# Kernel optimization log

Hardware: AMD Instinct MI355X
Metric: run time of the kernel (lower is better)

Reference implementation:

```python
import jax, jax.numpy as jnp
import numpy as np

B, N, D, H = 8, 1024, 512, 8
DK = D // H  # key_dim == val_dim == 64
LN_EPS = 1e-5


def setup_inputs() -> dict:
    key = jax.random.key(0)
    ks = jax.random.split(key, 16)
    stdv = 1.0 / np.sqrt(D)
    u = lambda k, shape, s: jax.random.uniform(k, shape, jnp.float32, -s, s)
    inp = {
        'q': jax.random.normal(ks[0], (B, N, D), jnp.float32),
        'mask': jax.random.uniform(ks[1], (B, N, N)) < 0.1,  # True = masked out
        # eps1 is torch.zeros in the source (never re-initialized); use small
        'eps1': jax.random.normal(ks[2], (D, D), jnp.float32) * 0.03,
        # 3 MLP layers, stacked on leading axis. Linear: y = x @ W.T + b
        'U_w': u(ks[3], (3, D, D), stdv), 'U_b': u(ks[4], (3, D), stdv),
        'V_w': u(ks[5], (3, D, D), stdv), 'V_b': u(ks[6], (3, D), stdv),
        'ln_g': jnp.ones((3, D), jnp.float32), 'ln_b': jnp.zeros((3, D), jnp.float32),
        'W_query': u(ks[7], (H, D, DK), 1.0 / np.sqrt(DK)),
        'W_key':   u(ks[8], (H, D, DK), 1.0 / np.sqrt(DK)),
        'W_val':   u(ks[9], (H, D, DK), 1.0 / np.sqrt(DK)),
        'W_out':   u(ks[10], (H, DK, D), stdv),
    }
    return inp


def _layer_norm(x, g, b):
    mu = jnp.mean(x, axis=-1, keepdims=True)
    var = jnp.mean(jnp.square(x - mu), axis=-1, keepdims=True)
    return (x - mu) * jax.lax.rsqrt(var + LN_EPS) * g + b


def _mlp_layer(x, Uw, Ub, Vw, Vb, g, b):
    # U1 -> (identity maxpool k=1) -> V1 -> LayerNorm -> ReLU -> residual
    y = x @ Uw.T + Ub
    y = y @ Vw.T + Vb
    y = _layer_norm(y, g, b)
    return x + jax.nn.relu(y)


def reference(q, mask, eps1, U_w, U_b, V_w, V_b, ln_g, ln_b,
              W_query, W_key, W_val, W_out):
    nf = 1.0 / np.sqrt(DK)  # norm_factor; applied to BOTH Q and K as in source
    h = q
    for l in range(3):
        h = _mlp_layer(h @ eps1, U_w[l], U_b[l], V_w[l], V_b[l], ln_g[l], ln_b[l])
    # per-head projections: (H,B,N,DK)
    Q = jnp.einsum('bqd,hdk->hbqk', q, W_query) * nf
    K = jnp.einsum('bgd,hdk->hbgk', h, W_key) * nf
    V = jnp.einsum('bgd,hdk->hbgk', h, W_val)
    scores = jnp.einsum('hbqk,hbgk->hbqg', Q, K)  # (H,B,N,N)
    scores = jnp.where(mask[None], -1e10, scores)
    attn = jax.nn.softmax(scores, axis=-1)
    heads = jnp.einsum('hbqg,hbgv->hbqv', attn, V)
    out = jnp.einsum('hbqv,hvd->bqd', heads, W_out)  # (B,N,D)
    return out
```

## Files before the change

kernel.cpp:

```cpp
#include <hip/hip_runtime.h>

typedef __attribute__((ext_vector_type(8))) short bhalf8;
typedef __attribute__((ext_vector_type(4))) float f32x4;

__device__ __forceinline__ ushort f2bf(float f) {
  unsigned u = __builtin_bit_cast(unsigned, f);
  unsigned r = u + 0x7fffu + ((u >> 16) & 1u);
  return (ushort)(r >> 16);
}

__device__ __forceinline__ void gld16(const ushort* g, ushort* l) {
  __builtin_amdgcn_global_load_lds((const __attribute__((address_space(1))) void*)g,
                                   (__attribute__((address_space(3))) void*)l, 16, 0, 0);
}

__global__ __launch_bounds__(256) void prep_kernel(
    const float* __restrict__ q, const int* __restrict__ mask,
    const float* __restrict__ eps1, const float* __restrict__ U_w,
    const float* __restrict__ V_w, const float* __restrict__ Wq,
    const float* __restrict__ Wk, const float* __restrict__ Wv,
    const float* __restrict__ Wo, const float* __restrict__ U_b,
    const float* __restrict__ V_b,
    ushort* __restrict__ qb, unsigned long long* __restrict__ mbits,
    ushort* __restrict__ uwb, ushort* __restrict__ vwb,
    ushort* __restrict__ e1b, ushort* __restrict__ e1t,
    ushort* __restrict__ wqkv, ushort* __restrict__ wot,
    float* __restrict__ cvec) {
  int i = blockIdx.x * 256 + threadIdx.x;
  if (i < 4194304) {
    qb[i] = f2bf(q[i]);
  } else if (i < 12582912) {
    int j = i - 4194304;
    unsigned long long bb = __ballot(mask[j] != 0);
    if ((threadIdx.x & 63) == 0) {
      int b = j >> 20, qq = (j >> 10) & 1023, g = j & 1023;
      mbits[((size_t)b * 16 + (g >> 6)) * 1024 + qq] = bb;
    }
  } else if (i < 13369344) {
    int j = i - 12582912;
    uwb[j] = f2bf(U_w[j]);
  } else if (i < 14155776) {
    int j = i - 13369344;
    vwb[j] = f2bf(V_w[j]);
  } else if (i < 14417920) {
    int j = i - 14155776;
    e1b[j] = f2bf(eps1[j]);
  } else if (i < 14680064) {
    int j = i - 14417920; int n = j >> 9, k = j & 511;
    e1t[j] = f2bf(eps1[k * 512 + n]);
  } else if (i < 15466496) {
    int j = i - 14680064; int n = j >> 9, d = j & 511;
    const float* W = (n < 512) ? Wq : (n < 1024 ? Wk : Wv);
    float sc = (n < 512) ? 0.02255252509f : 1.0f;
    int nl = n & 511;
    wqkv[j] = f2bf(W[((nl >> 6) * 512 + d) * 64 + (nl & 63)] * sc);
  } else if (i < 15728640) {
    int j = i - 15466496; int d = j >> 9, hv = j & 511;
    wot[j] = f2bf(Wo[hv * 512 + d]);
  } else {
    int j = i - 15728640;
    int idx = j >> 6, ln = j & 63;
    int l = idx >> 9;
    const float* vr = V_w + (size_t)idx * 512 + ln * 8;
    const float* ur = U_b + l * 512 + ln * 8;
    float s = 0;
#pragma unroll
    for (int t = 0; t < 8; t++) s += vr[t] * ur[t];
#pragma unroll
    for (int off = 1; off < 64; off <<= 1) s += __shfl_xor(s, off, 64);
    if (ln == 0) cvec[idx] = s + V_b[idx];
  }
}

__global__ __launch_bounds__(256) void mrepack_kernel(
    const unsigned long long* __restrict__ mbits,
    unsigned long long* __restrict__ mT) {
  int id = blockIdx.x * 4 + (threadIdx.x >> 6);
  int lane = threadIdx.x & 63;
  int b = id >> 8, gw = (id >> 4) & 15, qw = id & 15;
  unsigned long long row = mbits[((size_t)b * 16 + gw) * 1024 + qw * 64 + lane];
  unsigned long long keep = 0;
  for (int j = 0; j < 64; j++) {
    unsigned long long bal = __ballot((row >> j) & 1ull);
    if (lane == j) keep = bal;
  }
  mT[((size_t)b * 1024 + gw * 64 + lane) * 16 + qw] = keep;
}

template <int BN>
__global__ __launch_bounds__(256) void gemm_nt(
    const ushort* __restrict__ A0, const ushort* __restrict__ A1,
    const ushort* __restrict__ Bt0, const ushort* __restrict__ Bt1,
    int bsplit, int mstride, int M, int K,
    ushort* __restrict__ O0, const float* __restrict__ b0,
    ushort* __restrict__ O1, const float* __restrict__ b1,
    ushort* __restrict__ O2, const float* __restrict__ b2,
    float* __restrict__ F0, float* __restrict__ F1, int vtreg) {
  __shared__ ushort As[128 * 32];
  __shared__ ushort Bs[BN * 32];
  int tid = threadIdx.x;
  int wave = tid >> 6, lane = tid & 63;
  int quad = lane >> 4, col = lane & 15;
  int m0 = blockIdx.x * 128, n0 = blockIdx.y * BN;
  const ushort* A = (A1 && n0 >= 512) ? A1 : A0;
  const ushort* Bp = ((n0 < bsplit) ? Bt0 + (size_t)n0 * K
                                    : Bt1 + (size_t)(n0 - bsplit) * K) +
                     (size_t)(m0 >> 9) * mstride;
  constexpr int NI = BN / 32;
  int wm = (BN == 128) ? (wave >> 1) * 64 : (wave & 1) * 64;
  int wn = (BN == 128) ? (wave & 1) * 64 : (wave >> 1) * 32;
  f32x4 acc[4][NI] = {};
  int srow = wave * 16 + (lane >> 2);
  int skc = (lane & 3) * 8;
  const ushort* gA0 = A + (size_t)(m0 + srow) * K + skc;
  const ushort* gA1 = gA0 + (size_t)64 * K;
  const ushort* gB0 = Bp + (size_t)srow * K + skc;
  const ushort* gB1 = gB0 + (size_t)64 * K;
  ushort* lA0 = &As[wave * 16 * 32];
  ushort* lA1 = &As[(64 + wave * 16) * 32];
  ushort* lB0 = &Bs[wave * 16 * 32];
  ushort* lB1 = (BN == 128) ? &Bs[(64 + wave * 16) * 32] : nullptr;

  gld16(gA0, lA0);
  gld16(gA1, lA1);
  gld16(gB0, lB0);
  if (BN == 128) gld16(gB1, lB1);

  for (int k0 = 0; k0 < K; k0 += 32) {
    __syncthreads();
    bhalf8 af[4], bg[NI];
#pragma unroll
    for (int i = 0; i < 4; i++)
      af[i] = *(bhalf8*)&As[(wm + i * 16 + col) * 32 + quad * 8];
#pragma unroll
    for (int i = 0; i < NI; i++)
      bg[i] = *(bhalf8*)&Bs[(wn + i * 16 + col) * 32 + quad * 8];
    __syncthreads();
    if (k0 + 32 < K) {
      gld16(gA0 + k0 + 32, lA0);
      gld16(gA1 + k0 + 32, lA1);
      gld16(gB0 + k0 + 32, lB0);
      if (BN == 128) gld16(gB1 + k0 + 32, lB1);
    }
#pragma unroll
    for (int mi = 0; mi < 4; mi++)
#pragma unroll
      for (int ni = 0; ni < NI; ni++)
        acc[mi][ni] = __builtin_amdgcn_mfma_f32_16x16x32_bf16(af[mi], bg[ni], acc[mi][ni], 0, 0, 0);
  }

  int reg = n0 >> 9;
  ushort* Oreg = (reg == 0) ? O0 : (reg == 1 ? O1 : O2);
  const float* breg = (reg == 0) ? b0 : (reg == 1 ? b1 : b2);
  float* Freg = (reg == 0) ? F0 : (reg == 1 ? F1 : nullptr);
  bool vt = (reg == vtreg);
#pragma unroll
  for (int mi = 0; mi < 4; mi++)
#pragma unroll
    for (int ni = 0; ni < NI; ni++) {
      int cn = n0 + wn + ni * 16 + col;
      int cnl = cn & 511;
      int cmb = m0 + wm + mi * 16 + quad * 4;
      float bv = breg ? breg[cnl] : 0.f;
      if (vt) {
        ushort4 pk;
        pk.x = f2bf(acc[mi][ni][0] + bv);
        pk.y = f2bf(acc[mi][ni][1] + bv);
        pk.z = f2bf(acc[mi][ni][2] + bv);
        pk.w = f2bf(acc[mi][ni][3] + bv);
        *(ushort4*)&O2[((size_t)((cmb >> 10) * 512 + cnl)) * 1024 + (cmb & 1023)] = pk;
      } else if (Freg) {
#pragma unroll
        for (int r = 0; r < 4; r++)
          Freg[(size_t)(cmb + r) * 512 + cnl] = acc[mi][ni][r] + bv;
      } else {
#pragma unroll
        for (int r = 0; r < 4; r++)
          Oreg[(size_t)(cmb + r) * 512 + cnl] = f2bf(acc[mi][ni][r] + bv);
      }
    }
}

__global__ __launch_bounds__(256) void ln_kernel(
    const float* __restrict__ z, const ushort* __restrict__ tb,
    const float* __restrict__ lgam, const float* __restrict__ lbet,
    ushort* __restrict__ hb) {
  int row = blockIdx.x * 4 + (threadIdx.x >> 6);
  int lane = threadIdx.x & 63;
  int cbase = lane * 8;
  const float* zr = z + (size_t)row * 512 + cbase;
  float x[8];
  *(float4*)&x[0] = *(const float4*)zr;
  *(float4*)&x[4] = *(const float4*)(zr + 4);
  float sum = 0;
#pragma unroll
  for (int i = 0; i < 8; i++) sum += x[i];
#pragma unroll
  for (int off = 1; off < 64; off <<= 1) sum += __shfl_xor(sum, off, 64);
  float mu = sum * (1.f / 512.f);
  float vs = 0;
#pragma unroll
  for (int i = 0; i < 8; i++) { float d = x[i] - mu; vs += d * d; }
#pragma unroll
  for (int off = 1; off < 64; off <<= 1) vs += __shfl_xor(vs, off, 64);
  float rstd = rsqrtf(vs * (1.f / 512.f) + 1e-5f);
  uint4 tr = *(const uint4*)&tb[(size_t)row * 512 + cbase];
  float tv[8];
  {
    const unsigned* u = (const unsigned*)&tr;
#pragma unroll
    for (int w = 0; w < 4; w++) {
      tv[2 * w] = __builtin_bit_cast(float, u[w] << 16);
      tv[2 * w + 1] = __builtin_bit_cast(float, u[w] & 0xFFFF0000u);
    }
  }
  ushort outv[8];
#pragma unroll
  for (int i = 0; i < 8; i++) {
    float val = (x[i] - mu) * rstd * lgam[cbase + i] + lbet[cbase + i];
    outv[i] = f2bf(tv[i] + fmaxf(val, 0.f));
  }
  *(uint4*)&hb[(size_t)row * 512 + cbase] = *(uint4*)outv;
}

__global__ __launch_bounds__(256, 2) void attn_kernel(
    const ushort* __restrict__ Qp, const ushort* __restrict__ Kp,
    const ushort* __restrict__ VtG, const unsigned long long* __restrict__ mT,
    ushort* __restrict__ Op) {
  int bh = blockIdx.x, qt = blockIdx.y;
  int b = bh >> 3, h = bh & 7;
  __shared__ __align__(16) char pool[21504];
  int tid = threadIdx.x, wave = tid >> 6, lane = tid & 63;
  int quad = lane >> 4, col = lane & 15;
  int q0 = qt * 64;
  ushort* Ps = (ushort*)pool + wave * 2560;

  bhalf8 aq[4][2];
  {
    const ushort* qbase = &Qp[(size_t)(b * 1024 + q0 + col) * 512 + h * 64 + quad * 8];
#pragma unroll
    for (int qs = 0; qs < 4; qs++) {
      aq[qs][0] = *(const bhalf8*)(qbase + (size_t)(qs * 16) * 512);
      aq[qs][1] = *(const bhalf8*)(qbase + (size_t)(qs * 16) * 512 + 32);
    }
  }
  bhalf8 ones;
  {
    short v = (col == 0) ? (short)0x3F80 : (short)0;
#pragma unroll
    for (int j = 0; j < 8; j++) ones[j] = v;
  }
  f32x4 o[4][5] = {};
  const ushort* kbase = &Kp[(size_t)(b * 1024 + col) * 512 + h * 64 + quad * 8];
  const ushort* vbase = &VtG[(size_t)(bh * 64 + col) * 1024];
  int gsel = (quad >> 1) * 64 + (quad & 1) * 8;

  for (int g0 = 0; g0 < 1024; g0 += 128) {
    int gA = g0 + wave * 16;
    bhalf8 bk[2][2];
    bk[0][0] = *(const bhalf8*)(kbase + (size_t)gA * 512);
    bk[0][1] = *(const bhalf8*)(kbase + (size_t)gA * 512 + 32);
    bk[1][0] = *(const bhalf8*)(kbase + (size_t)(gA + 64) * 512);
    bk[1][1] = *(const bhalf8*)(kbase + (size_t)(gA + 64) * 512 + 32);
    bhalf8 bv[4];
#pragma unroll
    for (int vs = 0; vs < 4; vs++)
      bv[vs] = *(const bhalf8*)(vbase + (size_t)(vs * 16) * 1024 + g0 + wave * 16 + gsel);
    unsigned long long inv0 = ~(mT[(size_t)(b * 1024 + gA + col) * 16 + qt] >> (quad * 4));
    unsigned long long inv1 = ~(mT[(size_t)(b * 1024 + gA + 64 + col) * 16 + qt] >> (quad * 4));
    unsigned i0lo = (unsigned)inv0, i0hi = (unsigned)(inv0 >> 32);
    unsigned i1lo = (unsigned)inv1, i1hi = (unsigned)(inv1 >> 32);
#pragma unroll
    for (int qs = 0; qs < 4; qs++) {
      f32x4 s0 = {}, s1 = {};
      s0 = __builtin_amdgcn_mfma_f32_16x16x32_bf16(aq[qs][0], bk[0][0], s0, 0, 0, 0);
      s0 = __builtin_amdgcn_mfma_f32_16x16x32_bf16(aq[qs][1], bk[0][1], s0, 0, 0, 0);
      s1 = __builtin_amdgcn_mfma_f32_16x16x32_bf16(aq[qs][0], bk[1][0], s1, 0, 0, 0);
      s1 = __builtin_amdgcn_mfma_f32_16x16x32_bf16(aq[qs][1], bk[1][1], s1, 0, 0, 0);
      unsigned w0 = (qs < 2) ? i0lo : i0hi;
      unsigned w1 = (qs < 2) ? i1lo : i1hi;
#pragma unroll
      for (int r = 0; r < 4; r++) {
        int pos = (qs & 1) * 16 + r;
        unsigned k0 = (unsigned)((int)(w0 << (31 - pos)) >> 31);
        unsigned k1 = (unsigned)((int)(w1 << (31 - pos)) >> 31);
        unsigned p0 = __builtin_bit_cast(unsigned, __builtin_amdgcn_exp2f(s0[r])) & k0;
        unsigned p1 = __builtin_bit_cast(unsigned, __builtin_amdgcn_exp2f(s1[r])) & k1;
        Ps[(qs * 16 + quad * 4 + r) * 40 + col] = (ushort)((p0 + 0x8000u) >> 16);
        Ps[(qs * 16 + quad * 4 + r) * 40 + 16 + col] = (ushort)((p1 + 0x8000u) >> 16);
      }
    }
#pragma unroll
    for (int qs = 0; qs < 4; qs++) {
      bhalf8 ap = *(const bhalf8*)&Ps[(qs * 16 + col) * 40 + quad * 8];
#pragma unroll
      for (int vs = 0; vs < 4; vs++)
        o[qs][vs] = __builtin_amdgcn_mfma_f32_16x16x32_bf16(ap, bv[vs], o[qs][vs], 0, 0, 0);
      o[qs][4] = __builtin_amdgcn_mfma_f32_16x16x32_bf16(ap, ones, o[qs][4], 0, 0, 0);
    }
  }
  float* R = (float*)pool;
  for (int src = 1; src < 4; src++) {
    __syncthreads();
    if (wave == src) {
      float* dst = R + lane * 84;
#pragma unroll
      for (int qs = 0; qs < 4; qs++)
#pragma unroll
        for (int vs = 0; vs < 5; vs++)
          *(f32x4*)(dst + (qs * 5 + vs) * 4) = o[qs][vs];
    }
    __syncthreads();
    if (wave == 0) {
      const float* sp = R + lane * 84;
#pragma unroll
      for (int qs = 0; qs < 4; qs++)
#pragma unroll
        for (int vs = 0; vs < 5; vs++)
          o[qs][vs] += *(const f32x4*)(sp + (qs * 5 + vs) * 4);
    }
  }
  if (wave == 0) {
#pragma unroll
    for (int qs = 0; qs < 4; qs++) {
      float rl[4];
#pragma unroll
      for (int r = 0; r < 4; r++) {
        float lv = __shfl(o[qs][4][r], lane & 48, 64);
        rl[r] = __builtin_amdgcn_rcpf(lv);
      }
#pragma unroll
      for (int vs = 0; vs < 4; vs++)
#pragma unroll
        for (int r = 0; r < 4; r++) {
          int qrow = q0 + qs * 16 + quad * 4 + r;
          Op[(size_t)(b * 1024 + qrow) * 512 + h * 64 + vs * 16 + col] =
              f2bf(o[qs][vs][r] * rl[r]);
        }
    }
  }
}

extern "C" void kernel_launch(void* const* d_in, const int* in_sizes, int n_in,
                              void* d_out, int out_size, void* d_ws, size_t ws_size,
                              hipStream_t stream) {
  const float* q    = (const float*)d_in[0];
  const int*   mask = (const int*)d_in[1];
  const float* eps1 = (const float*)d_in[2];
  const float* U_w  = (const float*)d_in[3];
  const float* U_b  = (const float*)d_in[4];
  const float* V_w  = (const float*)d_in[5];
  const float* V_b  = (const float*)d_in[6];
  const float* ln_g = (const float*)d_in[7];
  const float* ln_b = (const float*)d_in[8];
  const float* Wq   = (const float*)d_in[9];
  const float* Wk   = (const float*)d_in[10];
  const float* Wv   = (const float*)d_in[11];
  const float* Wo   = (const float*)d_in[12];
  float* out = (float*)d_out;

  char* ws = (char*)d_ws;
  auto carve = [&](size_t bytes) { char* p = ws; ws += bytes; return p; };
  ushort* qb   = (ushort*)carve(8388608);
  ushort* uwb  = (ushort*)carve(1572864);
  ushort* vwb  = (ushort*)carve(1572864);
  ushort* e1b  = (ushort*)carve(524288);
  ushort* e1t  = (ushort*)carve(524288);
  ushort* wqkv = (ushort*)carve(1572864);
  ushort* wot  = (ushort*)carve(524288);
  ushort* A1b  = (ushort*)carve(1572864);
  ushort* Gtb  = (ushort*)carve(1572864);
  float*  cvec = (float*)carve(6144);
  unsigned long long* mbits = (unsigned long long*)carve(1048576);
  unsigned long long* mT    = (unsigned long long*)carve(2097152);
  ushort* tb   = (ushort*)carve(8388608);
  float*  zf   = (float*)carve(16777216);
  ushort* hb   = (ushort*)carve(8388608);
  ushort* Qb   = (ushort*)carve(8388608);
  ushort* Kb   = (ushort*)carve(8388608);
  ushort* VtG  = (ushort*)carve(8388608);
  ushort* Ob   = (ushort*)carve(8388608);
  const int BIG = 1 << 30;

  prep_kernel<<<61824, 256, 0, stream>>>(q, mask, eps1, U_w, V_w, Wq, Wk, Wv, Wo,
                                         U_b, V_b, qb, mbits, uwb, vwb, e1b, e1t,
                                         wqkv, wot, cvec);
  mrepack_kernel<<<512, 256, 0, stream>>>(mbits, mT);
  gemm_nt<128><<<dim3(4, 12), 256, 0, stream>>>(
      e1b, nullptr, uwb, nullptr, BIG, 0, 512, 512,
      A1b, nullptr, A1b + 262144, nullptr, A1b + 524288, nullptr,
      nullptr, nullptr, -1);
  gemm_nt<64><<<dim3(12, 8), 256, 0, stream>>>(
      vwb, nullptr, A1b, nullptr, BIG, 262144, 1536, 512,
      Gtb, nullptr, nullptr, nullptr, nullptr, nullptr,
      nullptr, nullptr, -1);
  const ushort* hsrc = qb;
  for (int l = 0; l < 3; l++) {
    gemm_nt<128><<<dim3(64, 8), 256, 0, stream>>>(
        hsrc, nullptr, e1t, Gtb + l * 262144, 512, 0, 8192, 512,
        tb, nullptr, nullptr, cvec + l * 512, nullptr, nullptr,
        nullptr, zf, -1);
    ln_kernel<<<2048, 256, 0, stream>>>(zf, tb, ln_g + l * 512, ln_b + l * 512, hb);
    hsrc = hb;
  }
  gemm_nt<128><<<dim3(64, 12), 256, 0, stream>>>(
      qb, hb, wqkv, nullptr, BIG, 0, 8192, 512,
      Qb, nullptr, Kb, nullptr, VtG, nullptr, nullptr, nullptr, 2);
  attn_kernel<<<dim3(64, 16), 256, 0, stream>>>(Qb, Kb, VtG, mT, Ob);
  gemm_nt<64><<<dim3(64, 8), 256, 0, stream>>>(
      Ob, nullptr, wot, nullptr, BIG, 0, 8192, 512,
      nullptr, nullptr, nullptr, nullptr, nullptr, nullptr, out, nullptr, -1);
}
```

Before: 318.5 us.

## Tile K/V/mask layouts for attention and widen GEMM k-step to 64

The GEMM epilogue now writes K and V directly into per-(batch,head) 16-row tiled layouts, so the attention kernel's fragment loads become contiguous per wave instead of strided across 512-wide rows. The mask repack stores pre-inverted bits in a q-tile-major layout to shrink and linearize the mask reads. The GEMM main loop moves to a 64-wide k-step with double the LDS tile, halving the barrier and issue count per K. Scattered epilogue stores for K and the larger LDS footprint are the trade-offs.

Result: no change. 321.4 us (+0.9%).

```diff
diff --git a/kernel.cpp b/kernel.cpp
--- a/kernel.cpp
+++ b/kernel.cpp
@@ -74,7 +74,7 @@
 
 __global__ __launch_bounds__(256) void mrepack_kernel(
     const unsigned long long* __restrict__ mbits,
-    unsigned long long* __restrict__ mT) {
+    unsigned long long* __restrict__ mT2) {
   int id = blockIdx.x * 4 + (threadIdx.x >> 6);
   int lane = threadIdx.x & 63;
   int b = id >> 8, gw = (id >> 4) & 15, qw = id & 15;
@@ -84,7 +84,7 @@
     unsigned long long bal = __ballot((row >> j) & 1ull);
     if (lane == j) keep = bal;
   }
-  mT[((size_t)b * 1024 + gw * 64 + lane) * 16 + qw] = keep;
+  mT2[((size_t)b * 16 + qw) * 1024 + gw * 64 + lane] = ~keep;
 }
 
 template <int BN>
@@ -95,9 +95,10 @@
     ushort* __restrict__ O0, const float* __restrict__ b0,
     ushort* __restrict__ O1, const float* __restrict__ b1,
     ushort* __restrict__ O2, const float* __restrict__ b2,
-    float* __restrict__ F0, float* __restrict__ F1, int vtreg) {
-  __shared__ ushort As[128 * 32];
-  __shared__ ushort Bs[BN * 32];
+    float* __restrict__ F0, float* __restrict__ F1,
+    int ktreg, int vtreg) {
+  __shared__ ushort As[128 * 64];
+  __shared__ ushort Bs[BN * 64];
   int tid = threadIdx.x;
   int wave = tid >> 6, lane = tid & 63;
   int quad = lane >> 4, col = lane & 15;
@@ -110,50 +111,72 @@
   int wm = (BN == 128) ? (wave >> 1) * 64 : (wave & 1) * 64;
   int wn = (BN == 128) ? (wave & 1) * 64 : (wave >> 1) * 32;
   f32x4 acc[4][NI] = {};
-  int srow = wave * 16 + (lane >> 2);
-  int skc = (lane & 3) * 8;
-  const ushort* gA0 = A + (size_t)(m0 + srow) * K + skc;
-  const ushort* gA1 = gA0 + (size_t)64 * K;
-  const ushort* gB0 = Bp + (size_t)srow * K + skc;
-  const ushort* gB1 = gB0 + (size_t)64 * K;
-  ushort* lA0 = &As[wave * 16 * 32];
-  ushort* lA1 = &As[(64 + wave * 16) * 32];
-  ushort* lB0 = &Bs[wave * 16 * 32];
-  ushort* lB1 = (BN == 128) ? &Bs[(64 + wave * 16) * 32] : nullptr;
-
-  gld16(gA0, lA0);
-  gld16(gA1, lA1);
-  gld16(gB0, lB0);
-  if (BN == 128) gld16(gB1, lB1);
-
-  for (int k0 = 0; k0 < K; k0 += 32) {
+  int srow = wave * 16 + (lane >> 3);
+  int skc = (lane & 7) * 8;
+  const ushort* gA = A + (size_t)(m0 + srow) * K + skc;
+  const ushort* gB = Bp + (size_t)srow * K + skc;
+  ushort* lA = &As[(wave * 16) * 64];
+  ushort* lB = &Bs[(wave * 16) * 64];
+  const size_t rK8 = (size_t)8 * K, rK64 = (size_t)64 * K;
+
+  gld16(gA, lA);
+  gld16(gA + rK8, lA + 8 * 64);
+  gld16(gA + rK64, lA + 64 * 64);
+  gld16(gA + rK64 + rK8, lA + 72 * 64);
+  gld16(gB, lB);
+  gld16(gB + rK8, lB + 8 * 64);
+  if (BN == 128) {
+    gld16(gB + rK64, lB + 64 * 64);
+    gld16(gB + rK64 + rK8, lB + 72 * 64);
+  }
+
+  for (int k0 = 0; k0 < K; k0 += 64) {
     __syncthreads();
     bhalf8 af[4], bg[NI];
 #pragma unroll
     for (int i = 0; i < 4; i++)
-      af[i] = *(bhalf8*)&As[(wm + i * 16 + col) * 32 + quad * 8];
+      af[i] = *(bhalf8*)&As[(wm + i * 16 + col) * 64 + quad * 8];
 #pragma unroll
     for (int i = 0; i < NI; i++)
-      bg[i] = *(bhalf8*)&Bs[(wn + i * 16 + col) * 32 + quad * 8];
-    __syncthreads();
-    if (k0 + 32 < K) {
-      gld16(gA0 + k0 + 32, lA0);
-      gld16(gA1 + k0 + 32, lA1);
-      gld16(gB0 + k0 + 32, lB0);
-      if (BN == 128) gld16(gB1 + k0 + 32, lB1);
-    }
+      bg[i] = *(bhalf8*)&Bs[(wn + i * 16 + col) * 64 + quad * 8];
 #pragma unroll
     for (int mi = 0; mi < 4; mi++)
 #pragma unroll
       for (int ni = 0; ni < NI; ni++)
         acc[mi][ni] = __builtin_amdgcn_mfma_f32_16x16x32_bf16(af[mi], bg[ni], acc[mi][ni], 0, 0, 0);
+    bhalf8 af2[4], bg2[NI];
+#pragma unroll
+    for (int i = 0; i < 4; i++)
+      af2[i] = *(bhalf8*)&As[(wm + i * 16 + col) * 64 + 32 + quad * 8];
+#pragma unroll
+    for (int i = 0; i < NI; i++)
+      bg2[i] = *(bhalf8*)&Bs[(wn + i * 16 + col) * 64 + 32 + quad * 8];
+    __syncthreads();
+    if (k0 + 64 < K) {
+      const ushort* a = gA + k0 + 64;
+      const ushort* b = gB + k0 + 64;
+      gld16(a, lA);
+      gld16(a + rK8, lA + 8 * 64);
+      gld16(a + rK64, lA + 64 * 64);
+      gld16(a + rK64 + rK8, lA + 72 * 64);
+      gld16(b, lB);
+      gld16(b + rK8, lB + 8 * 64);
+      if (BN == 128) {
+        gld16(b + rK64, lB + 64 * 64);
+        gld16(b + rK64 + rK8, lB + 72 * 64);
+      }
+    }
+#pragma unroll
+    for (int mi = 0; mi < 4; mi++)
+#pragma unroll
+      for (int ni = 0; ni < NI; ni++)
+        acc[mi][ni] = __builtin_amdgcn_mfma_f32_16x16x32_bf16(af2[mi], bg2[ni], acc[mi][ni], 0, 0, 0);
   }
 
   int reg = n0 >> 9;
   ushort* Oreg = (reg == 0) ? O0 : (reg == 1 ? O1 : O2);
   const float* breg = (reg == 0) ? b0 : (reg == 1 ? b1 : b2);
   float* Freg = (reg == 0) ? F0 : (reg == 1 ? F1 : nullptr);
-  bool vt = (reg == vtreg);
 #pragma unroll
   for (int mi = 0; mi < 4; mi++)
 #pragma unroll
@@ -161,22 +184,32 @@
       int cn = n0 + wn + ni * 16 + col;
       int cnl = cn & 511;
       int cmb = m0 + wm + mi * 16 + quad * 4;
-      float bv = breg ? breg[cnl] : 0.f;
-      if (vt) {
+      float bvv = breg ? breg[cnl] : 0.f;
+      if (reg == vtreg) {
+        int bhh = (cmb >> 10) * 8 + (cnl >> 6);
+        size_t base = ((size_t)bhh * 64 + ((cmb & 1023) >> 4)) * 1024 +
+                      (size_t)(cnl & 63) * 16 + (cmb & 15);
         ushort4 pk;
-        pk.x = f2bf(acc[mi][ni][0] + bv);
-        pk.y = f2bf(acc[mi][ni][1] + bv);
-        pk.z = f2bf(acc[mi][ni][2] + bv);
-        pk.w = f2bf(acc[mi][ni][3] + bv);
-        *(ushort4*)&O2[((size_t)((cmb >> 10) * 512 + cnl)) * 1024 + (cmb & 1023)] = pk;
+        pk.x = f2bf(acc[mi][ni][0] + bvv);
+        pk.y = f2bf(acc[mi][ni][1] + bvv);
+        pk.z = f2bf(acc[mi][ni][2] + bvv);
+        pk.w = f2bf(acc[mi][ni][3] + bvv);
+        *(ushort4*)&Oreg[base] = pk;
+      } else if (reg == ktreg) {
+        int bhh = (cmb >> 10) * 8 + (cnl >> 6);
+        size_t base = ((size_t)bhh * 64 + ((cmb & 1023) >> 4)) * 1024 +
+                      (size_t)((cnl >> 5) & 1) * 512 + (size_t)(cmb & 15) * 32 + (cnl & 31);
+#pragma unroll
+        for (int r = 0; r < 4; r++)
+          Oreg[base + r * 32] = f2bf(acc[mi][ni][r] + bvv);
       } else if (Freg) {
 #pragma unroll
         for (int r = 0; r < 4; r++)
-          Freg[(size_t)(cmb + r) * 512 + cnl] = acc[mi][ni][r] + bv;
+          Freg[(size_t)(cmb + r) * 512 + cnl] = acc[mi][ni][r] + bvv;
       } else {
 #pragma unroll
         for (int r = 0; r < 4; r++)
-          Oreg[(size_t)(cmb + r) * 512 + cnl] = f2bf(acc[mi][ni][r] + bv);
+          Oreg[(size_t)(cmb + r) * 512 + cnl] = f2bf(acc[mi][ni][r] + bvv);
       }
     }
 }
@@ -224,8 +257,8 @@
 }
 
 __global__ __launch_bounds__(256, 2) void attn_kernel(
-    const ushort* __restrict__ Qp, const ushort* __restrict__ Kp,
-    const ushort* __restrict__ VtG, const unsigned long long* __restrict__ mT,
+    const ushort* __restrict__ Qp, const ushort* __restrict__ KtT,
+    const ushort* __restrict__ VtT, const unsigned long long* __restrict__ mT2,
     ushort* __restrict__ Op) {
   int bh = blockIdx.x, qt = blockIdx.y;
   int b = bh >> 3, h = bh & 7;
@@ -251,25 +284,26 @@
     for (int j = 0; j < 8; j++) ones[j] = v;
   }
   f32x4 o[4][5] = {};
-  const ushort* kbase = &Kp[(size_t)(b * 1024 + col) * 512 + h * 64 + quad * 8];
-  const ushort* vbase = &VtG[(size_t)(bh * 64 + col) * 1024];
-  int gsel = (quad >> 1) * 64 + (quad & 1) * 8;
+  const ushort* kbase = KtT + (size_t)bh * 65536 + wave * 1024 + col * 32 + quad * 8;
+  const ushort* vbase = VtT + (size_t)bh * 65536 + wave * 1024 + (quad >> 1) * 4096 +
+                        col * 16 + (quad & 1) * 8;
+  const unsigned long long* mbase = &mT2[((size_t)b * 16 + qt) * 1024 + wave * 16 + col];
 
   for (int g0 = 0; g0 < 1024; g0 += 128) {
-    int gA = g0 + wave * 16;
+    int goff = g0 * 64;
     bhalf8 bk[2][2];
-    bk[0][0] = *(const bhalf8*)(kbase + (size_t)gA * 512);
-    bk[0][1] = *(const bhalf8*)(kbase + (size_t)gA * 512 + 32);
-    bk[1][0] = *(const bhalf8*)(kbase + (size_t)(gA + 64) * 512);
-    bk[1][1] = *(const bhalf8*)(kbase + (size_t)(gA + 64) * 512 + 32);
+    bk[0][0] = *(const bhalf8*)(kbase + goff);
+    bk[0][1] = *(const bhalf8*)(kbase + goff + 512);
+    bk[1][0] = *(const bhalf8*)(kbase + goff + 4096);
+    bk[1][1] = *(const bhalf8*)(kbase + goff + 4096 + 512);
     bhalf8 bv[4];
 #pragma unroll
     for (int vs = 0; vs < 4; vs++)
-      bv[vs] = *(const bhalf8*)(vbase + (size_t)(vs * 16) * 1024 + g0 + wave * 16 + gsel);
-    unsigned long long inv0 = ~(mT[(size_t)(b * 1024 + gA + col) * 16 + qt] >> (quad * 4));
-    unsigned long long inv1 = ~(mT[(size_t)(b * 1024 + gA + 64 + col) * 16 + qt] >> (quad * 4));
-    unsigned i0lo = (unsigned)inv0, i0hi = (unsigned)(inv0 >> 32);
-    unsigned i1lo = (unsigned)inv1, i1hi = (unsigned)(inv1 >> 32);
+      bv[vs] = *(const bhalf8*)(vbase + goff + vs * 256);
+    unsigned long long i64_0 = mbase[g0] >> (quad * 4);
+    unsigned long long i64_1 = mbase[g0 + 64] >> (quad * 4);
+    unsigned i0lo = (unsigned)i64_0, i0hi = (unsigned)(i64_0 >> 32);
+    unsigned i1lo = (unsigned)i64_1, i1hi = (unsigned)(i64_1 >> 32);
 #pragma unroll
     for (int qs = 0; qs < 4; qs++) {
       f32x4 s0 = {}, s1 = {};
@@ -372,42 +406,42 @@
   ushort* Gtb  = (ushort*)carve(1572864);
   float*  cvec = (float*)carve(6144);
   unsigned long long* mbits = (unsigned long long*)carve(1048576);
-  unsigned long long* mT    = (unsigned long long*)carve(2097152);
+  unsigned long long* mT2   = (unsigned long long*)carve(1048576);
   ushort* tb   = (ushort*)carve(8388608);
   float*  zf   = (float*)carve(16777216);
   ushort* hb   = (ushort*)carve(8388608);
   ushort* Qb   = (ushort*)carve(8388608);
-  ushort* Kb   = (ushort*)carve(8388608);
-  ushort* VtG  = (ushort*)carve(8388608);
+  ushort* Ktt  = (ushort*)carve(8388608);
+  ushort* Vtt  = (ushort*)carve(8388608);
   ushort* Ob   = (ushort*)carve(8388608);
   const int BIG = 1 << 30;
 
   prep_kernel<<<61824, 256, 0, stream>>>(q, mask, eps1, U_w, V_w, Wq, Wk, Wv, Wo,
                                          U_b, V_b, qb, mbits, uwb, vwb, e1b, e1t,
                                          wqkv, wot, cvec);
-  mrepack_kernel<<<512, 256, 0, stream>>>(mbits, mT);
+  mrepack_kernel<<<512, 256, 0, stream>>>(mbits, mT2);
   gemm_nt<128><<<dim3(4, 12), 256, 0, stream>>>(
       e1b, nullptr, uwb, nullptr, BIG, 0, 512, 512,
       A1b, nullptr, A1b + 262144, nullptr, A1b + 524288, nullptr,
-      nullptr, nullptr, -1);
+      nullptr, nullptr, -1, -1);
   gemm_nt<64><<<dim3(12, 8), 256, 0, stream>>>(
       vwb, nullptr, A1b, nullptr, BIG, 262144, 1536, 512,
       Gtb, nullptr, nullptr, nullptr, nullptr, nullptr,
-      nullptr, nullptr, -1);
+      nullptr, nullptr, -1, -1);
   const ushort* hsrc = qb;
   for (int l = 0; l < 3; l++) {
     gemm_nt<128><<<dim3(64, 8), 256, 0, stream>>>(
         hsrc, nullptr, e1t, Gtb + l * 262144, 512, 0, 8192, 512,
         tb, nullptr, nullptr, cvec + l * 512, nullptr, nullptr,
-        nullptr, zf, -1);
+        nullptr, zf, -1, -1);
     ln_kernel<<<2048, 256, 0, stream>>>(zf, tb, ln_g + l * 512, ln_b + l * 512, hb);
     hsrc = hb;
   }
   gemm_nt<128><<<dim3(64, 12), 256, 0, stream>>>(
       qb, hb, wqkv, nullptr, BIG, 0, 8192, 512,
-      Qb, nullptr, Kb, nullptr, VtG, nullptr, nullptr, nullptr, 2);
-  attn_kernel<<<dim3(64, 16), 256, 0, stream>>>(Qb, Kb, VtG, mT, Ob);
+      Qb, nullptr, Ktt, nullptr, Vtt, nullptr, nullptr, nullptr, 1, 2);
+  attn_kernel<<<dim3(64, 16), 256, 0, stream>>>(Qb, Ktt, Vtt, mT2, Ob);
   gemm_nt<64><<<dim3(64, 8), 256, 0, stream>>>(
       Ob, nullptr, wot, nullptr, BIG, 0, 8192, 512,
-      nullptr, nullptr, nullptr, nullptr, nullptr, nullptr, out, nullptr, -1);
-}
+      nullptr, nullptr, nullptr, nullptr, nullptr, nullptr, out, nullptr, -1, -1);
+}
```

## Tile Q/K/V into MFMA-friendly blocks and compute attention transposed, dropping mask repack

Applied to the files above, without the earlier changes.

The QKV projection GEMM now writes Q, K and V in per-(batch,head) 16-row tiled layouts that match the MFMA operand fragments. The attention kernel computes scores as K·Qᵀ, so the exp'd probabilities are already in the B-operand layout of a 16x16x16 MFMA. This removes the per-wave LDS staging of P and the extra ones-column MFMA for row sums, which are now kept in registers. The mask is stored inverted straight from the prep kernel, so the separate mask transpose kernel goes away, and occupancy is raised to 3 blocks per SM. The cost is smaller-K MFMAs for the PV product and more complex scatter-style GEMM epilogue stores.

Measured after the change: 308.4 us. 3.1% less time.

```diff
diff --git a/kernel.cpp b/kernel.cpp
--- a/kernel.cpp
+++ b/kernel.cpp
@@ -1,6 +1,7 @@
 #include <hip/hip_runtime.h>
 
 typedef __attribute__((ext_vector_type(8))) short bhalf8;
+typedef __attribute__((ext_vector_type(4))) short bhalf4;
 typedef __attribute__((ext_vector_type(4))) float f32x4;
 
 __device__ __forceinline__ ushort f2bf(float f) {
@@ -21,7 +22,7 @@
     const float* __restrict__ Wk, const float* __restrict__ Wv,
     const float* __restrict__ Wo, const float* __restrict__ U_b,
     const float* __restrict__ V_b,
-    ushort* __restrict__ qb, unsigned long long* __restrict__ mbits,
+    ushort* __restrict__ qb, unsigned long long* __restrict__ minv,
     ushort* __restrict__ uwb, ushort* __restrict__ vwb,
     ushort* __restrict__ e1b, ushort* __restrict__ e1t,
     ushort* __restrict__ wqkv, ushort* __restrict__ wot,
@@ -34,7 +35,7 @@
     unsigned long long bb = __ballot(mask[j] != 0);
     if ((threadIdx.x & 63) == 0) {
       int b = j >> 20, qq = (j >> 10) & 1023, g = j & 1023;
-      mbits[((size_t)b * 16 + (g >> 6)) * 1024 + qq] = bb;
+      minv[((size_t)b * 16 + (g >> 6)) * 1024 + qq] = ~bb;
     }
   } else if (i < 13369344) {
     int j = i - 12582912;
@@ -72,30 +73,14 @@
   }
 }
 
-__global__ __launch_bounds__(256) void mrepack_kernel(
-    const unsigned long long* __restrict__ mbits,
-    unsigned long long* __restrict__ mT) {
-  int id = blockIdx.x * 4 + (threadIdx.x >> 6);
-  int lane = threadIdx.x & 63;
-  int b = id >> 8, gw = (id >> 4) & 15, qw = id & 15;
-  unsigned long long row = mbits[((size_t)b * 16 + gw) * 1024 + qw * 64 + lane];
-  unsigned long long keep = 0;
-  for (int j = 0; j < 64; j++) {
-    unsigned long long bal = __ballot((row >> j) & 1ull);
-    if (lane == j) keep = bal;
-  }
-  mT[((size_t)b * 1024 + gw * 64 + lane) * 16 + qw] = keep;
-}
-
 template <int BN>
 __global__ __launch_bounds__(256) void gemm_nt(
     const ushort* __restrict__ A0, const ushort* __restrict__ A1,
     const ushort* __restrict__ Bt0, const ushort* __restrict__ Bt1,
     int bsplit, int mstride, int M, int K,
-    ushort* __restrict__ O0, const float* __restrict__ b0,
-    ushort* __restrict__ O1, const float* __restrict__ b1,
-    ushort* __restrict__ O2, const float* __restrict__ b2,
-    float* __restrict__ F0, float* __restrict__ F1, int vtreg) {
+    ushort* __restrict__ Oa, const float* __restrict__ ba, int ca,
+    ushort* __restrict__ Ob, const float* __restrict__ bb2, int cb,
+    ushort* __restrict__ Oc, const float* __restrict__ bc, int cc) {
   __shared__ ushort As[128 * 32];
   __shared__ ushort Bs[BN * 32];
   int tid = threadIdx.x;
@@ -150,10 +135,9 @@
   }
 
   int reg = n0 >> 9;
-  ushort* Oreg = (reg == 0) ? O0 : (reg == 1 ? O1 : O2);
-  const float* breg = (reg == 0) ? b0 : (reg == 1 ? b1 : b2);
-  float* Freg = (reg == 0) ? F0 : (reg == 1 ? F1 : nullptr);
-  bool vt = (reg == vtreg);
+  ushort* O = (reg == 0) ? Oa : (reg == 1 ? Ob : Oc);
+  const float* bs = (reg == 0) ? ba : (reg == 1 ? bb2 : bc);
+  int code = (reg == 0) ? ca : (reg == 1 ? cb : cc);
 #pragma unroll
   for (int mi = 0; mi < 4; mi++)
 #pragma unroll
@@ -161,22 +145,33 @@
       int cn = n0 + wn + ni * 16 + col;
       int cnl = cn & 511;
       int cmb = m0 + wm + mi * 16 + quad * 4;
-      float bv = breg ? breg[cnl] : 0.f;
-      if (vt) {
+      float bv = bs ? bs[cnl] : 0.f;
+      if (code == 2) {
+        int bhh = (cmb >> 10) * 8 + (cnl >> 6);
+        size_t base = ((size_t)bhh * 64 + ((cmb & 1023) >> 4)) * 1024 +
+                      (size_t)((cnl >> 5) & 1) * 512 + (size_t)(cmb & 15) * 32 + (cnl & 31);
+#pragma unroll
+        for (int r = 0; r < 4; r++)
+          O[base + r * 32] = f2bf(acc[mi][ni][r] + bv);
+      } else if (code == 3) {
+        int bhh = (cmb >> 10) * 8 + (cnl >> 6);
+        size_t base = ((size_t)bhh * 64 + ((cmb & 1023) >> 4)) * 1024 +
+                      (size_t)(cnl & 63) * 16 + (cmb & 15);
         ushort4 pk;
         pk.x = f2bf(acc[mi][ni][0] + bv);
         pk.y = f2bf(acc[mi][ni][1] + bv);
         pk.z = f2bf(acc[mi][ni][2] + bv);
         pk.w = f2bf(acc[mi][ni][3] + bv);
-        *(ushort4*)&O2[((size_t)((cmb >> 10) * 512 + cnl)) * 1024 + (cmb & 1023)] = pk;
-      } else if (Freg) {
+        *(ushort4*)&O[base] = pk;
+      } else if (code == 1) {
+        float* Ff = (float*)O;
 #pragma unroll
         for (int r = 0; r < 4; r++)
-          Freg[(size_t)(cmb + r) * 512 + cnl] = acc[mi][ni][r] + bv;
+          Ff[(size_t)(cmb + r) * 512 + cnl] = acc[mi][ni][r] + bv;
       } else {
 #pragma unroll
         for (int r = 0; r < 4; r++)
-          Oreg[(size_t)(cmb + r) * 512 + cnl] = f2bf(acc[mi][ni][r] + bv);
+          O[(size_t)(cmb + r) * 512 + cnl] = f2bf(acc[mi][ni][r] + bv);
       }
     }
 }
@@ -223,121 +218,114 @@
   *(uint4*)&hb[(size_t)row * 512 + cbase] = *(uint4*)outv;
 }
 
-__global__ __launch_bounds__(256, 2) void attn_kernel(
-    const ushort* __restrict__ Qp, const ushort* __restrict__ Kp,
-    const ushort* __restrict__ VtG, const unsigned long long* __restrict__ mT,
+__global__ __launch_bounds__(256, 3) void attn_kernel(
+    const ushort* __restrict__ QtT, const ushort* __restrict__ KtT,
+    const ushort* __restrict__ VtT, const unsigned long long* __restrict__ minv,
     ushort* __restrict__ Op) {
-  int bh = blockIdx.x, qt = blockIdx.y;
+  int bh = blockIdx.x, qt0 = blockIdx.y;
   int b = bh >> 3, h = bh & 7;
-  __shared__ __align__(16) char pool[21504];
-  int tid = threadIdx.x, wave = tid >> 6, lane = tid & 63;
+  __shared__ float R[64 * 68];
+  int tid = threadIdx.x, w = tid >> 6, lane = tid & 63;
   int quad = lane >> 4, col = lane & 15;
-  int q0 = qt * 64;
-  ushort* Ps = (ushort*)pool + wave * 2560;
-
-  bhalf8 aq[4][2];
-  {
-    const ushort* qbase = &Qp[(size_t)(b * 1024 + q0 + col) * 512 + h * 64 + quad * 8];
-#pragma unroll
-    for (int qs = 0; qs < 4; qs++) {
-      aq[qs][0] = *(const bhalf8*)(qbase + (size_t)(qs * 16) * 512);
-      aq[qs][1] = *(const bhalf8*)(qbase + (size_t)(qs * 16) * 512 + 32);
-    }
-  }
-  bhalf8 ones;
-  {
-    short v = (col == 0) ? (short)0x3F80 : (short)0;
-#pragma unroll
-    for (int j = 0; j < 8; j++) ones[j] = v;
-  }
-  f32x4 o[4][5] = {};
-  const ushort* kbase = &Kp[(size_t)(b * 1024 + col) * 512 + h * 64 + quad * 8];
-  const ushort* vbase = &VtG[(size_t)(bh * 64 + col) * 1024];
-  int gsel = (quad >> 1) * 64 + (quad & 1) * 8;
+  int q0 = qt0 * 64;
+  const ushort* Kt = KtT + (size_t)bh * 65536 + col * 32 + quad * 8;
+  const ushort* Vt = VtT + (size_t)bh * 65536 + col * 16 + quad * 4;
+  const ushort* Qt = QtT + (size_t)bh * 65536 + col * 32 + quad * 8;
+  bhalf8 bq[4][2];
+#pragma unroll
+  for (int qt = 0; qt < 4; qt++)
+#pragma unroll
+    for (int ks = 0; ks < 2; ks++)
+      bq[qt][ks] = *(const bhalf8*)(Qt + (size_t)(qt0 * 4 + qt) * 1024 + ks * 512);
+  f32x4 o[4][4] = {};
+  float lsum[4] = {0.f, 0.f, 0.f, 0.f};
+  const unsigned long long* mb = minv + (size_t)b * 16384 + q0 + col;
 
   for (int g0 = 0; g0 < 1024; g0 += 128) {
-    int gA = g0 + wave * 16;
-    bhalf8 bk[2][2];
-    bk[0][0] = *(const bhalf8*)(kbase + (size_t)gA * 512);
-    bk[0][1] = *(const bhalf8*)(kbase + (size_t)gA * 512 + 32);
-    bk[1][0] = *(const bhalf8*)(kbase + (size_t)(gA + 64) * 512);
-    bk[1][1] = *(const bhalf8*)(kbase + (size_t)(gA + 64) * 512 + 32);
-    bhalf8 bv[4];
-#pragma unroll
-    for (int vs = 0; vs < 4; vs++)
-      bv[vs] = *(const bhalf8*)(vbase + (size_t)(vs * 16) * 1024 + g0 + wave * 16 + gsel);
-    unsigned long long inv0 = ~(mT[(size_t)(b * 1024 + gA + col) * 16 + qt] >> (quad * 4));
-    unsigned long long inv1 = ~(mT[(size_t)(b * 1024 + gA + 64 + col) * 16 + qt] >> (quad * 4));
-    unsigned i0lo = (unsigned)inv0, i0hi = (unsigned)(inv0 >> 32);
-    unsigned i1lo = (unsigned)inv1, i1hi = (unsigned)(inv1 >> 32);
-#pragma unroll
-    for (int qs = 0; qs < 4; qs++) {
-      f32x4 s0 = {}, s1 = {};
-      s0 = __builtin_amdgcn_mfma_f32_16x16x32_bf16(aq[qs][0], bk[0][0], s0, 0, 0, 0);
-      s0 = __builtin_amdgcn_mfma_f32_16x16x32_bf16(aq[qs][1], bk[0][1], s0, 0, 0, 0);
-      s1 = __builtin_amdgcn_mfma_f32_16x16x32_bf16(aq[qs][0], bk[1][0], s1, 0, 0, 0);
-      s1 = __builtin_amdgcn_mfma_f32_16x16x32_bf16(aq[qs][1], bk[1][1], s1, 0, 0, 0);
-      unsigned w0 = (qs < 2) ? i0lo : i0hi;
-      unsigned w1 = (qs < 2) ? i1lo : i1hi;
-#pragma unroll
-      for (int r = 0; r < 4; r++) {
-        int pos = (qs & 1) * 16 + r;
-        unsigned k0 = (unsigned)((int)(w0 << (31 - pos)) >> 31);
-        unsigned k1 = (unsigned)((int)(w1 << (31 - pos)) >> 31);
-        unsigned p0 = __builtin_bit_cast(unsigned, __builtin_amdgcn_exp2f(s0[r])) & k0;
-        unsigned p1 = __builtin_bit_cast(unsigned, __builtin_amdgcn_exp2f(s1[r])) & k1;
-        Ps[(qs * 16 + quad * 4 + r) * 40 + col] = (ushort)((p0 + 0x8000u) >> 16);
-        Ps[(qs * 16 + quad * 4 + r) * 40 + 16 + col] = (ushort)((p1 + 0x8000u) >> 16);
+    int gs = g0 + w * 32;
+    int gw = gs >> 6;
+    int sb = (gs & 32) + quad * 4;
+    unsigned shq[4];
+#pragma unroll
+    for (int qt = 0; qt < 4; qt++)
+      shq[qt] = (unsigned)(mb[gw * 1024 + qt * 16] >> sb);
+#pragma unroll
+    for (int gt = 0; gt < 2; gt++) {
+      size_t gblk = (size_t)((gs >> 4) + gt) * 1024;
+      bhalf8 ak0 = *(const bhalf8*)(Kt + gblk);
+      bhalf8 ak1 = *(const bhalf8*)(Kt + gblk + 512);
+      bhalf4 av[4];
+#pragma unroll
+      for (int vt = 0; vt < 4; vt++)
+        av[vt] = *(const bhalf4*)(Vt + gblk + vt * 256);
+#pragma unroll
+      for (int qt = 0; qt < 4; qt++) {
+        f32x4 s = {};
+        s = __builtin_amdgcn_mfma_f32_16x16x32_bf16(ak0, bq[qt][0], s, 0, 0, 0);
+        s = __builtin_amdgcn_mfma_f32_16x16x32_bf16(ak1, bq[qt][1], s, 0, 0, 0);
+        unsigned sh = shq[qt];
+        unsigned pu[4];
+#pragma unroll
+        for (int r = 0; r < 4; r++) {
+          const int pos = gt * 16 + r;
+          unsigned keep = (unsigned)((int)(sh << (31 - pos)) >> 31);
+          pu[r] = __builtin_bit_cast(unsigned, __builtin_amdgcn_exp2f(s[r])) & keep;
+          lsum[qt] += __builtin_bit_cast(float, pu[r]);
+        }
+        uint2 pp;
+        pp.x = ((pu[0] + 0x8000u) >> 16) | (((pu[1] + 0x8000u) >> 16) << 16);
+        pp.y = ((pu[2] + 0x8000u) >> 16) | (((pu[3] + 0x8000u) >> 16) << 16);
+        bhalf4 bp = __builtin_bit_cast(bhalf4, pp);
+#pragma unroll
+        for (int vt = 0; vt < 4; vt++)
+          o[vt][qt] = __builtin_amdgcn_mfma_f32_16x16x16bf16_1k(av[vt], bp, o[vt][qt], 0, 0, 0);
       }
     }
-#pragma unroll
-    for (int qs = 0; qs < 4; qs++) {
-      bhalf8 ap = *(const bhalf8*)&Ps[(qs * 16 + col) * 40 + quad * 8];
-#pragma unroll
-      for (int vs = 0; vs < 4; vs++)
-        o[qs][vs] = __builtin_amdgcn_mfma_f32_16x16x32_bf16(ap, bv[vs], o[qs][vs], 0, 0, 0);
-      o[qs][4] = __builtin_amdgcn_mfma_f32_16x16x32_bf16(ap, ones, o[qs][4], 0, 0, 0);
-    }
-  }
-  float* R = (float*)pool;
+  }
   for (int src = 1; src < 4; src++) {
     __syncthreads();
-    if (wave == src) {
-      float* dst = R + lane * 84;
-#pragma unroll
-      for (int qs = 0; qs < 4; qs++)
-#pragma unroll
-        for (int vs = 0; vs < 5; vs++)
-          *(f32x4*)(dst + (qs * 5 + vs) * 4) = o[qs][vs];
+    if (w == src) {
+      float* dst = R + lane * 68;
+#pragma unroll
+      for (int vt = 0; vt < 4; vt++)
+#pragma unroll
+        for (int qt = 0; qt < 4; qt++)
+          *(f32x4*)(dst + (vt * 4 + qt) * 4) = o[vt][qt];
+#pragma unroll
+      for (int qt = 0; qt < 4; qt++) dst[64 + qt] = lsum[qt];
     }
     __syncthreads();
-    if (wave == 0) {
-      const float* sp = R + lane * 84;
-#pragma unroll
-      for (int qs = 0; qs < 4; qs++)
-#pragma unroll
-        for (int vs = 0; vs < 5; vs++)
-          o[qs][vs] += *(const f32x4*)(sp + (qs * 5 + vs) * 4);
-    }
-  }
-  if (wave == 0) {
-#pragma unroll
-    for (int qs = 0; qs < 4; qs++) {
-      float rl[4];
-#pragma unroll
-      for (int r = 0; r < 4; r++) {
-        float lv = __shfl(o[qs][4][r], lane & 48, 64);
-        rl[r] = __builtin_amdgcn_rcpf(lv);
+    if (w == 0) {
+      const float* sp = R + lane * 68;
+#pragma unroll
+      for (int vt = 0; vt < 4; vt++)
+#pragma unroll
+        for (int qt = 0; qt < 4; qt++)
+          o[vt][qt] += *(const f32x4*)(sp + (vt * 4 + qt) * 4);
+#pragma unroll
+      for (int qt = 0; qt < 4; qt++) lsum[qt] += sp[64 + qt];
+    }
+  }
+  if (w == 0) {
+    float rl[4];
+#pragma unroll
+    for (int qt = 0; qt < 4; qt++) {
+      lsum[qt] += __shfl_xor(lsum[qt], 16, 64);
+      lsum[qt] += __shfl_xor(lsum[qt], 32, 64);
+      rl[qt] = __builtin_amdgcn_rcpf(lsum[qt]);
+    }
+#pragma unroll
+    for (int vt = 0; vt < 4; vt++)
+#pragma unroll
+      for (int qt = 0; qt < 4; qt++) {
+        ushort4 pk;
+        pk.x = f2bf(o[vt][qt][0] * rl[qt]);
+        pk.y = f2bf(o[vt][qt][1] * rl[qt]);
+        pk.z = f2bf(o[vt][qt][2] * rl[qt]);
+        pk.w = f2bf(o[vt][qt][3] * rl[qt]);
+        *(ushort4*)&Op[(size_t)(b * 1024 + q0 + qt * 16 + col) * 512 +
+                       h * 64 + vt * 16 + quad * 4] = pk;
       }
-#pragma unroll
-      for (int vs = 0; vs < 4; vs++)
-#pragma unroll
-        for (int r = 0; r < 4; r++) {
-          int qrow = q0 + qs * 16 + quad * 4 + r;
-          Op[(size_t)(b * 1024 + qrow) * 512 + h * 64 + vs * 16 + col] =
-              f2bf(o[qs][vs][r] * rl[r]);
-        }
-    }
   }
 }
 
@@ -371,43 +359,38 @@
   ushort* A1b  = (ushort*)carve(1572864);
   ushort* Gtb  = (ushort*)carve(1572864);
   float*  cvec = (float*)carve(6144);
-  unsigned long long* mbits = (unsigned long long*)carve(1048576);
-  unsigned long long* mT    = (unsigned long long*)carve(2097152);
+  unsigned long long* minv = (unsigned long long*)carve(1048576);
   ushort* tb   = (ushort*)carve(8388608);
   float*  zf   = (float*)carve(16777216);
   ushort* hb   = (ushort*)carve(8388608);
-  ushort* Qb   = (ushort*)carve(8388608);
-  ushort* Kb   = (ushort*)carve(8388608);
-  ushort* VtG  = (ushort*)carve(8388608);
+  ushort* Qtt  = (ushort*)carve(8388608);
+  ushort* Ktt  = (ushort*)carve(8388608);
+  ushort* Vtt  = (ushort*)carve(8388608);
   ushort* Ob   = (ushort*)carve(8388608);
   const int BIG = 1 << 30;
 
   prep_kernel<<<61824, 256, 0, stream>>>(q, mask, eps1, U_w, V_w, Wq, Wk, Wv, Wo,
-                                         U_b, V_b, qb, mbits, uwb, vwb, e1b, e1t,
+                                         U_b, V_b, qb, minv, uwb, vwb, e1b, e1t,
                                          wqkv, wot, cvec);
-  mrepack_kernel<<<512, 256, 0, stream>>>(mbits, mT);
   gemm_nt<128><<<dim3(4, 12), 256, 0, stream>>>(
       e1b, nullptr, uwb, nullptr, BIG, 0, 512, 512,
-      A1b, nullptr, A1b + 262144, nullptr, A1b + 524288, nullptr,
-      nullptr, nullptr, -1);
+      A1b, nullptr, 0, A1b + 262144, nullptr, 0, A1b + 524288, nullptr, 0);
   gemm_nt<64><<<dim3(12, 8), 256, 0, stream>>>(
       vwb, nullptr, A1b, nullptr, BIG, 262144, 1536, 512,
-      Gtb, nullptr, nullptr, nullptr, nullptr, nullptr,
-      nullptr, nullptr, -1);
+      Gtb, nullptr, 0, nullptr, nullptr, 0, nullptr, nullptr, 0);
   const ushort* hsrc = qb;
   for (int l = 0; l < 3; l++) {
     gemm_nt<128><<<dim3(64, 8), 256, 0, stream>>>(
         hsrc, nullptr, e1t, Gtb + l * 262144, 512, 0, 8192, 512,
-        tb, nullptr, nullptr, cvec + l * 512, nullptr, nullptr,
-        nullptr, zf, -1);
+        tb, nullptr, 0, (ushort*)zf, cvec + l * 512, 1, nullptr, nullptr, 0);
     ln_kernel<<<2048, 256, 0, stream>>>(zf, tb, ln_g + l * 512, ln_b + l * 512, hb);
     hsrc = hb;
   }
   gemm_nt<128><<<dim3(64, 12), 256, 0, stream>>>(
       qb, hb, wqkv, nullptr, BIG, 0, 8192, 512,
-      Qb, nullptr, Kb, nullptr, VtG, nullptr, nullptr, nullptr, 2);
-  attn_kernel<<<dim3(64, 16), 256, 0, stream>>>(Qb, Kb, VtG, mT, Ob);
+      Qtt, nullptr, 2, Ktt, nullptr, 2, Vtt, nullptr, 3);
+  attn_kernel<<<dim3(64, 16), 256, 0, stream>>>(Qtt, Ktt, Vtt, minv, Ob);
   gemm_nt<64><<<dim3(64, 8), 256, 0, stream>>>(
       Ob, nullptr, wot, nullptr, BIG, 0, 8192, 512,
-      nullptr, nullptr, nullptr, nullptr, nullptr, nullptr, out, nullptr, -1);
-}
+      (ushort*)out, nullptr, 1, nullptr, nullptr, 0, nullptr, nullptr, 0);
+}
```
